# Kernel optimization log

Hardware: AMD Instinct MI355X
Metric: run time of the kernel (lower is better)

Reference implementation:

```python
import jax, jax.numpy as jnp
import numpy as np


def setup_inputs() -> dict:
    key = jax.random.key(0)
    k1, k2, k3 = jax.random.split(key, 3)
    B, T, C, F = 32, 4096, 256, 256
    scale = 1.0 / np.sqrt(2 * C)  # glorot-ish fan-in scaling for kernel_size=2
    return {
        "x": jax.random.normal(k1, (B, T, C), dtype=jnp.float32),
        "Wv": jax.random.normal(k2, (2, C, F), dtype=jnp.float32) * scale,
        "bv": jnp.zeros((F,), dtype=jnp.float32),
        "Wg": jax.random.normal(k3, (2, C, F), dtype=jnp.float32) * scale,
        "bg": jnp.zeros((F,), dtype=jnp.float32),
        "dilation": 4,
    }


def _causal_dilated_k2(x, W, b, d):
    # Causal Conv1D, kernel_size=2, dilation d: y[t] = x[t-d] @ W[0] + x[t] @ W[1] + b
    T = x.shape[1]
    x_prev = jnp.pad(x, ((0, 0), (d, 0), (0, 0)))[:, :T]  # left-pad with zeros
    return (jnp.einsum("btc,cf->btf", x_prev, W[0])
            + jnp.einsum("btc,cf->btf", x, W[1]) + b)


def reference(x, Wv, bv, Wg, bg, dilation):
    value = jnp.tanh(_causal_dilated_k2(x, Wv, bv, dilation))
    gate = jax.nn.sigmoid(_causal_dilated_k2(x, Wg, bg, dilation))
    activations = value * gate
    # gate_merge = Concatenate (channel axis by default in Keras for 3D tensors)
    return jnp.concatenate([activations, x], axis=-1)
```

## Files before the change

### kernel.cpp

```cpp
#include <hip/hip_runtime.h>
#include <hip/hip_bf16.h>
#include <cstdint>

#define B_    32
#define T_    4096
#define C_    256
#define BM    64
#define DMAX  16
#define NROWS (BM + DMAX)

typedef __attribute__((ext_vector_type(8))) short bf16x8;
typedef __attribute__((ext_vector_type(4))) float f32x4;
typedef __attribute__((ext_vector_type(4))) short s16x4;

static __device__ __forceinline__ short f2bf(float f) {
  __hip_bfloat16 h = __float2bfloat16(f);
  union { __hip_bfloat16 h; short s; } u; u.h = h;
  return u.s;
}

static __device__ __forceinline__ float rcp_(float x) {
  return __builtin_amdgcn_rcpf(x);
}

__global__ void prep_weights(const float* __restrict__ Wv, const float* __restrict__ Wg,
                             const float* __restrict__ bv, const float* __restrict__ bg,
                             short* __restrict__ wimg, float* __restrict__ bcat) {
  int id = blockIdx.x * 256 + threadIdx.x;
  int kk = id & 31;
  int np = (id >> 5) & 255;
  int ks = (id >> 13) & 15;
  int nb = id >> 17;
  int k = ks * 32 + kk, tap = k >> 8, kr = k & 255;
  int sel = np >> 7;
  int f = nb * 128 + (np & 127);
  const float* W = sel ? Wg : Wv;
  wimg[id] = f2bf(W[((size_t)tap * 256 + kr) * 256 + f]);
  if (id < 512) bcat[id] = (id < 256) ? bv[id] : bg[id - 256];
}

__global__ __launch_bounds__(512, 4) void snail_main(
    const float* __restrict__ x, const short* __restrict__ wimg,
    const float* __restrict__ bcat, const int* __restrict__ dptr,
    float* __restrict__ out) {
  __shared__ __align__(16) short lx[NROWS * C_];

  const int d = *dptr;
  const int bid = blockIdx.x;
  const int swz = (bid & 7) * 256 + (bid >> 3);
  const int t0 = (swz & 63) * BM;
  const int b  = swz >> 6;

  const int tid  = threadIdx.x;
  const int lane = tid & 63;
  const int w    = tid >> 6;
  const int nb   = w >> 2;
  const int wq   = w & 3;
  const int row15 = lane & 15;
  const int qw    = lane >> 4;

  const float* xb = x + (size_t)b * T_ * C_;
  float* ob = out + (size_t)b * T_ * 512;

  for (int i = tid; i < d * 64; i += 512) {
    int r = i >> 6, c4 = i & 63;
    int t = t0 - d + r;
    f32x4 v = (f32x4){0.f, 0.f, 0.f, 0.f};
    if (t >= 0) v = *(const f32x4*)(xb + (size_t)t * C_ + c4 * 4);
    s16x4 s;
    s.x = f2bf(v.x); s.y = f2bf(v.y); s.z = f2bf(v.z); s.w = f2bf(v.w);
    int byte = (r * 512 + c4 * 8) ^ ((r & 7) << 4);
    *(s16x4*)((char*)lx + byte) = s;
  }
#pragma unroll 4
  for (int ii = 0; ii < 8; ++ii) {
    int i = ii * 512 + tid;
    int rr = i >> 6, c4 = i & 63;
    int t = t0 + rr, r = rr + d;
    f32x4 v = *(const f32x4*)(xb + (size_t)t * C_ + c4 * 4);
    __builtin_nontemporal_store(v, (f32x4*)(ob + (size_t)t * 512 + C_ + c4 * 4));
    s16x4 s;
    s.x = f2bf(v.x); s.y = f2bf(v.y); s.z = f2bf(v.z); s.w = f2bf(v.w);
    int byte = (r * 512 + c4 * 8) ^ ((r & 7) << 4);
    *(s16x4*)((char*)lx + byte) = s;
  }
  __syncthreads();

  f32x4 accv[4][2], accg[4][2];
#pragma unroll
  for (int mi = 0; mi < 4; ++mi)
#pragma unroll
    for (int ni = 0; ni < 2; ++ni) {
      accv[mi][ni] = (f32x4){0.f, 0.f, 0.f, 0.f};
      accg[mi][ni] = (f32x4){0.f, 0.f, 0.f, 0.f};
    }

  const short* wl = wimg + (size_t)nb * 131072 + (wq * 32 + row15) * 32 + qw * 8;

#define LOADW(D0, D1, D2, D3, KS) do {                                  \
    const short* wk_ = wl + (KS) * 8192;                                \
    D0 = *(const bf16x8*)(wk_);                                         \
    D1 = *(const bf16x8*)(wk_ + 512);                                   \
    D2 = *(const bf16x8*)(wk_ + 4096);                                  \
    D3 = *(const bf16x8*)(wk_ + 4608);                                  \
  } while (0)

#define STEP(B0, B1, G0, G1, KS) do {                                   \
    bf16x8 af[4];                                                       \
    const int rofs_ = ((KS) >= 8) ? d : 0;                              \
    const int cb_ = ((KS) & 7) * 64 + qw * 16;                          \
    _Pragma("unroll")                                                   \
    for (int mi = 0; mi < 4; ++mi) {                                    \
      int r_ = 16 * mi + row15 + rofs_;                                 \
      af[mi] = *(const bf16x8*)((const char*)lx +                       \
               ((r_ * 512 + cb_) ^ ((r_ & 7) << 4)));                   \
    }                                                                   \
    _Pragma("unroll")                                                   \
    for (int mi = 0; mi < 4; ++mi) {                                    \
      accv[mi][0] = __builtin_amdgcn_mfma_f32_16x16x32_bf16(B0, af[mi], accv[mi][0], 0, 0, 0); \
      accv[mi][1] = __builtin_amdgcn_mfma_f32_16x16x32_bf16(B1, af[mi], accv[mi][1], 0, 0, 0); \
      accg[mi][0] = __builtin_amdgcn_mfma_f32_16x16x32_bf16(G0, af[mi], accg[mi][0], 0, 0, 0); \
      accg[mi][1] = __builtin_amdgcn_mfma_f32_16x16x32_bf16(G1, af[mi], accg[mi][1], 0, 0, 0); \
    }                                                                   \
  } while (0)

  bf16x8 a0, a1, a2, a3, b0, b1, b2, b3;
  LOADW(a0, a1, a2, a3, 0);
#pragma unroll 1
  for (int ks2 = 0; ks2 < 8; ++ks2) {
    LOADW(b0, b1, b2, b3, 2 * ks2 + 1);
    STEP(a0, a1, a2, a3, 2 * ks2);
    if (ks2 < 7) LOADW(a0, a1, a2, a3, 2 * ks2 + 2);
    STEP(b0, b1, b2, b3, 2 * ks2 + 1);
  }
#undef LOADW
#undef STEP

#pragma unroll
  for (int ni = 0; ni < 2; ++ni) {
    int f0 = nb * 128 + wq * 32 + 16 * ni + qw * 4;
    f32x4 bv4 = *(const f32x4*)(bcat + f0);
    f32x4 bg4 = *(const f32x4*)(bcat + 256 + f0);
    f32x4 bv2 = bv4 + bv4;
    f32x4 bgn = -bg4;
#pragma unroll
    for (int mi = 0; mi < 4; ++mi) {
      int t = t0 + 16 * mi + row15;
      f32x4 v = accv[mi][ni], g = accg[mi][ni];
      f32x4 res;
#pragma unroll
      for (int j = 0; j < 4; ++j) {
        float e2v = __expf(__builtin_fmaf(v[j], 2.f, bv2[j]));
        float eng = __expf(__builtin_fmaf(g[j], -1.f, bgn[j]));
        res[j] = (e2v - 1.f) * rcp_((e2v + 1.f) * (1.f + eng));
      }
      __builtin_nontemporal_store(res, (f32x4*)(ob + (size_t)t * 512 + f0));
    }
  }
}

extern "C" void kernel_launch(void* const* d_in, const int* in_sizes, int n_in,
                              void* d_out, int out_size, void* d_ws, size_t ws_size,
                              hipStream_t stream) {
  const float* x  = (const float*)d_in[0];
  const float* Wv = (const float*)d_in[1];
  const float* bv = (const float*)d_in[2];
  const float* Wg = (const float*)d_in[3];
  const float* bg = (const float*)d_in[4];
  const int* dil  = (const int*)d_in[5];
  float* out = (float*)d_out;

  short* wimg = (short*)d_ws;
  float* bcat = (float*)((char*)d_ws + 16 * 32768);

  prep_weights<<<1024, 256, 0, stream>>>(Wv, Wg, bv, bg, wimg, bcat);
  snail_main<<<B_ * (T_ / BM), 512, 0, stream>>>(x, wimg, bcat, dil, out);
}
```

Before: 110.4 us.

## Switch GEMM to 32x32x16 MFMA with per-wave 32-feature slices

Replaces the 16x16x32 bf16 MFMA tiling with 32x32x16 MFMA. Each of the 8 waves now owns 32 value and 32 gate features across all 64 time rows. The weight image is re-laid out to match the new fragment layout, and the K loop now runs 32 steps of 16. The goal is fewer MFMA instructions and fewer LDS A-fragment loads per FLOP. The cost is a different LDS access pattern and a changed epilogue write layout, which may cause more bank conflicts or less coalesced stores.

Result: slower. 173.1 us (+56.9%).

```diff
diff --git a/kernel.cpp b/kernel.cpp
--- a/kernel.cpp
+++ b/kernel.cpp
@@ -9,9 +9,10 @@
 #define DMAX  16
 #define NROWS (BM + DMAX)
 
-typedef __attribute__((ext_vector_type(8))) short bf16x8;
-typedef __attribute__((ext_vector_type(4))) float f32x4;
-typedef __attribute__((ext_vector_type(4))) short s16x4;
+typedef __attribute__((ext_vector_type(8)))  short bf16x8;
+typedef __attribute__((ext_vector_type(4)))  float f32x4;
+typedef __attribute__((ext_vector_type(16))) float f32x16;
+typedef __attribute__((ext_vector_type(4)))  short s16x4;
 
 static __device__ __forceinline__ short f2bf(float f) {
   __hip_bfloat16 h = __float2bfloat16(f);
@@ -27,13 +28,15 @@
                              const float* __restrict__ bv, const float* __restrict__ bg,
                              short* __restrict__ wimg, float* __restrict__ bcat) {
   int id = blockIdx.x * 256 + threadIdx.x;
-  int kk = id & 31;
-  int np = (id >> 5) & 255;
-  int ks = (id >> 13) & 15;
-  int nb = id >> 17;
-  int k = ks * 32 + kk, tap = k >> 8, kr = k & 255;
-  int sel = np >> 7;
-  int f = nb * 128 + (np & 127);
+  int j     = id & 7;
+  int lane6 = (id >> 3) & 63;
+  int blk   = (id >> 9) & 15;
+  int ks    = id >> 13;
+  int f5 = lane6 & 31, hi = lane6 >> 5;
+  int k = ks * 16 + hi * 8 + j;
+  int tap = k >> 8, kr = k & 255;
+  int sel = blk >> 3;
+  int f = (blk & 7) * 32 + f5;
   const float* W = sel ? Wg : Wv;
   wimg[id] = f2bf(W[((size_t)tap * 256 + kr) * 256 + f]);
   if (id < 512) bcat[id] = (id < 256) ? bv[id] : bg[id - 256];
@@ -54,10 +57,9 @@
   const int tid  = threadIdx.x;
   const int lane = tid & 63;
   const int w    = tid >> 6;
-  const int nb   = w >> 2;
-  const int wq   = w & 3;
-  const int row15 = lane & 15;
-  const int qw    = lane >> 4;
+  const int l31  = lane & 31;
+  const int hi   = lane >> 5;
+  const int hi16 = hi * 16;
 
   const float* xb = x + (size_t)b * T_ * C_;
   float* ob = out + (size_t)b * T_ * 512;
@@ -86,72 +88,64 @@
   }
   __syncthreads();
 
-  f32x4 accv[4][2], accg[4][2];
+  f32x16 accv[2], accg[2];
 #pragma unroll
-  for (int mi = 0; mi < 4; ++mi)
-#pragma unroll
-    for (int ni = 0; ni < 2; ++ni) {
-      accv[mi][ni] = (f32x4){0.f, 0.f, 0.f, 0.f};
-      accg[mi][ni] = (f32x4){0.f, 0.f, 0.f, 0.f};
-    }
+  for (int mi = 0; mi < 2; ++mi) {
+    accv[mi] = (f32x16)(0.f);
+    accg[mi] = (f32x16)(0.f);
+  }
 
-  const short* wl = wimg + (size_t)nb * 131072 + (wq * 32 + row15) * 32 + qw * 8;
+  const short* wbase = wimg + lane * 8;
 
-#define LOADW(D0, D1, D2, D3, KS) do {                                  \
-    const short* wk_ = wl + (KS) * 8192;                                \
-    D0 = *(const bf16x8*)(wk_);                                         \
-    D1 = *(const bf16x8*)(wk_ + 512);                                   \
-    D2 = *(const bf16x8*)(wk_ + 4096);                                  \
-    D3 = *(const bf16x8*)(wk_ + 4608);                                  \
+#define LOADW(WV, WG, KS) do {                                          \
+    WV = *(const bf16x8*)(wbase + (size_t)((KS) * 16 + w) * 512);       \
+    WG = *(const bf16x8*)(wbase + (size_t)((KS) * 16 + 8 + w) * 512);   \
   } while (0)
 
-#define STEP(B0, B1, G0, G1, KS) do {                                   \
-    bf16x8 af[4];                                                       \
-    const int rofs_ = ((KS) >= 8) ? d : 0;                              \
-    const int cb_ = ((KS) & 7) * 64 + qw * 16;                          \
+#define STEP(WV, WG, KS) do {                                           \
+    bf16x8 af[2];                                                       \
+    const int rofs_ = ((KS) >= 16) ? d : 0;                             \
+    const int cb_ = ((KS) & 15) * 32 + hi16;                            \
     _Pragma("unroll")                                                   \
-    for (int mi = 0; mi < 4; ++mi) {                                    \
-      int r_ = 16 * mi + row15 + rofs_;                                 \
+    for (int mi = 0; mi < 2; ++mi) {                                    \
+      int r_ = 32 * mi + l31 + rofs_;                                   \
       af[mi] = *(const bf16x8*)((const char*)lx +                       \
                ((r_ * 512 + cb_) ^ ((r_ & 7) << 4)));                   \
     }                                                                   \
     _Pragma("unroll")                                                   \
-    for (int mi = 0; mi < 4; ++mi) {                                    \
-      accv[mi][0] = __builtin_amdgcn_mfma_f32_16x16x32_bf16(B0, af[mi], accv[mi][0], 0, 0, 0); \
-      accv[mi][1] = __builtin_amdgcn_mfma_f32_16x16x32_bf16(B1, af[mi], accv[mi][1], 0, 0, 0); \
-      accg[mi][0] = __builtin_amdgcn_mfma_f32_16x16x32_bf16(G0, af[mi], accg[mi][0], 0, 0, 0); \
-      accg[mi][1] = __builtin_amdgcn_mfma_f32_16x16x32_bf16(G1, af[mi], accg[mi][1], 0, 0, 0); \
+    for (int mi = 0; mi < 2; ++mi) {                                    \
+      accv[mi] = __builtin_amdgcn_mfma_f32_32x32x16_bf16(WV, af[mi], accv[mi], 0, 0, 0); \
+      accg[mi] = __builtin_amdgcn_mfma_f32_32x32x16_bf16(WG, af[mi], accg[mi], 0, 0, 0); \
     }                                                                   \
   } while (0)
 
-  bf16x8 a0, a1, a2, a3, b0, b1, b2, b3;
-  LOADW(a0, a1, a2, a3, 0);
+  bf16x8 av, ag, bv_, bg_;
+  LOADW(av, ag, 0);
 #pragma unroll 1
-  for (int ks2 = 0; ks2 < 8; ++ks2) {
-    LOADW(b0, b1, b2, b3, 2 * ks2 + 1);
-    STEP(a0, a1, a2, a3, 2 * ks2);
-    if (ks2 < 7) LOADW(a0, a1, a2, a3, 2 * ks2 + 2);
-    STEP(b0, b1, b2, b3, 2 * ks2 + 1);
+  for (int ks2 = 0; ks2 < 16; ++ks2) {
+    LOADW(bv_, bg_, 2 * ks2 + 1);
+    STEP(av, ag, 2 * ks2);
+    if (ks2 < 15) LOADW(av, ag, 2 * ks2 + 2);
+    STEP(bv_, bg_, 2 * ks2 + 1);
   }
 #undef LOADW
 #undef STEP
 
 #pragma unroll
-  for (int ni = 0; ni < 2; ++ni) {
-    int f0 = nb * 128 + wq * 32 + 16 * ni + qw * 4;
-    f32x4 bv4 = *(const f32x4*)(bcat + f0);
-    f32x4 bg4 = *(const f32x4*)(bcat + 256 + f0);
-    f32x4 bv2 = bv4 + bv4;
-    f32x4 bgn = -bg4;
+  for (int mi = 0; mi < 2; ++mi) {
+    int t = t0 + 32 * mi + l31;
 #pragma unroll
-    for (int mi = 0; mi < 4; ++mi) {
-      int t = t0 + 16 * mi + row15;
-      f32x4 v = accv[mi][ni], g = accg[mi][ni];
+    for (int rg = 0; rg < 4; ++rg) {
+      int f0 = 32 * w + rg * 8 + 4 * hi;
+      f32x4 bv4 = *(const f32x4*)(bcat + f0);
+      f32x4 bg4 = *(const f32x4*)(bcat + 256 + f0);
       f32x4 res;
 #pragma unroll
       for (int j = 0; j < 4; ++j) {
-        float e2v = __expf(__builtin_fmaf(v[j], 2.f, bv2[j]));
-        float eng = __expf(__builtin_fmaf(g[j], -1.f, bgn[j]));
+        float vv = accv[mi][rg * 4 + j];
+        float gg = accg[mi][rg * 4 + j];
+        float e2v = __expf(__builtin_fmaf(vv, 2.f, bv4[j] + bv4[j]));
+        float eng = __expf(__builtin_fmaf(gg, -1.f, -bg4[j]));
         res[j] = (e2v - 1.f) * rcp_((e2v + 1.f) * (1.f + eng));
       }
       __builtin_nontemporal_store(res, (f32x4*)(ob + (size_t)t * 512 + f0));
```

## Warp-specialize loader waves to double-buffer x tiles across four time tiles

Applied to the files above, without the earlier changes.

Each block now handles four consecutive 64-row time tiles with 768 threads. Four extra waves stage the next tile's x (bf16 into LDS plus the fp32 passthrough copy) into a second LDS buffer while eight compute waves run the MFMA GEMM and gated activation on the current buffer. The aim is to hide global load latency behind compute and amortize per-block setup. In exchange DMAX drops to 8, which breaks dilations above 8. Per-tile barriers couple the producer and consumer waves, and the grid shrinks to 512 blocks, which may reduce occupancy.

Result: slower. 122.3 us (+10.8%).

```diff
diff --git a/kernel.cpp b/kernel.cpp
--- a/kernel.cpp
+++ b/kernel.cpp
@@ -6,8 +6,9 @@
 #define T_    4096
 #define C_    256
 #define BM    64
-#define DMAX  16
+#define DMAX  8
 #define NROWS (BM + DMAX)
+#define NT    4
 
 typedef __attribute__((ext_vector_type(8))) short bf16x8;
 typedef __attribute__((ext_vector_type(4))) float f32x4;
@@ -39,63 +40,50 @@
   if (id < 512) bcat[id] = (id < 256) ? bv[id] : bg[id - 256];
 }
 
-__global__ __launch_bounds__(512, 4) void snail_main(
+__global__ __launch_bounds__(768, 3) void snail_main(
     const float* __restrict__ x, const short* __restrict__ wimg,
     const float* __restrict__ bcat, const int* __restrict__ dptr,
     float* __restrict__ out) {
-  __shared__ __align__(16) short lx[NROWS * C_];
+  __shared__ __align__(16) short lx[2][NROWS * C_];
 
   const int d = *dptr;
   const int bid = blockIdx.x;
-  const int swz = (bid & 7) * 256 + (bid >> 3);
-  const int t0 = (swz & 63) * BM;
-  const int b  = swz >> 6;
+  const int swz = (bid & 7) * 64 + (bid >> 3);
+  const int b   = swz >> 4;
+  const int t00 = (swz & 15) * (NT * BM);
 
   const int tid  = threadIdx.x;
   const int lane = tid & 63;
   const int w    = tid >> 6;
-  const int nb   = w >> 2;
-  const int wq   = w & 3;
-  const int row15 = lane & 15;
-  const int qw    = lane >> 4;
 
   const float* xb = x + (size_t)b * T_ * C_;
   float* ob = out + (size_t)b * T_ * 512;
 
-  for (int i = tid; i < d * 64; i += 512) {
+  const int nrows = BM + d;
+
+  for (int i = tid; i < nrows * 64; i += 768) {
     int r = i >> 6, c4 = i & 63;
-    int t = t0 - d + r;
+    int t = t00 - d + r;
     f32x4 v = (f32x4){0.f, 0.f, 0.f, 0.f};
     if (t >= 0) v = *(const f32x4*)(xb + (size_t)t * C_ + c4 * 4);
+    if (r >= d)
+      __builtin_nontemporal_store(v, (f32x4*)(ob + (size_t)t * 512 + C_ + c4 * 4));
     s16x4 s;
     s.x = f2bf(v.x); s.y = f2bf(v.y); s.z = f2bf(v.z); s.w = f2bf(v.w);
     int byte = (r * 512 + c4 * 8) ^ ((r & 7) << 4);
-    *(s16x4*)((char*)lx + byte) = s;
-  }
-#pragma unroll 4
-  for (int ii = 0; ii < 8; ++ii) {
-    int i = ii * 512 + tid;
-    int rr = i >> 6, c4 = i & 63;
-    int t = t0 + rr, r = rr + d;
-    f32x4 v = *(const f32x4*)(xb + (size_t)t * C_ + c4 * 4);
-    __builtin_nontemporal_store(v, (f32x4*)(ob + (size_t)t * 512 + C_ + c4 * 4));
-    s16x4 s;
-    s.x = f2bf(v.x); s.y = f2bf(v.y); s.z = f2bf(v.z); s.w = f2bf(v.w);
-    int byte = (r * 512 + c4 * 8) ^ ((r & 7) << 4);
-    *(s16x4*)((char*)lx + byte) = s;
+    *(s16x4*)((char*)&lx[0][0] + byte) = s;
   }
   __syncthreads();
 
-  f32x4 accv[4][2], accg[4][2];
-#pragma unroll
-  for (int mi = 0; mi < 4; ++mi)
-#pragma unroll
-    for (int ni = 0; ni < 2; ++ni) {
-      accv[mi][ni] = (f32x4){0.f, 0.f, 0.f, 0.f};
-      accg[mi][ni] = (f32x4){0.f, 0.f, 0.f, 0.f};
-    }
-
-  const short* wl = wimg + (size_t)nb * 131072 + (wq * 32 + row15) * 32 + qw * 8;
+  if (w < 8) {
+    const int nb   = w >> 2;
+    const int wq   = w & 3;
+    const int row15 = lane & 15;
+    const int qw    = lane >> 4;
+
+    const short* wl = wimg + (size_t)nb * 131072 + (wq * 32 + row15) * 32 + qw * 8;
+
+    f32x4 accv[4][2], accg[4][2];
 
 #define LOADW(D0, D1, D2, D3, KS) do {                                  \
     const short* wk_ = wl + (KS) * 8192;                                \
@@ -105,14 +93,14 @@
     D3 = *(const bf16x8*)(wk_ + 4608);                                  \
   } while (0)
 
-#define STEP(B0, B1, G0, G1, KS) do {                                   \
+#define STEP(BASE, B0, B1, G0, G1, KS) do {                             \
     bf16x8 af[4];                                                       \
     const int rofs_ = ((KS) >= 8) ? d : 0;                              \
     const int cb_ = ((KS) & 7) * 64 + qw * 16;                          \
     _Pragma("unroll")                                                   \
     for (int mi = 0; mi < 4; ++mi) {                                    \
       int r_ = 16 * mi + row15 + rofs_;                                 \
-      af[mi] = *(const bf16x8*)((const char*)lx +                       \
+      af[mi] = *(const bf16x8*)((BASE) +                                \
                ((r_ * 512 + cb_) ^ ((r_ & 7) << 4)));                   \
     }                                                                   \
     _Pragma("unroll")                                                   \
@@ -124,37 +112,76 @@
     }                                                                   \
   } while (0)
 
-  bf16x8 a0, a1, a2, a3, b0, b1, b2, b3;
-  LOADW(a0, a1, a2, a3, 0);
 #pragma unroll 1
-  for (int ks2 = 0; ks2 < 8; ++ks2) {
-    LOADW(b0, b1, b2, b3, 2 * ks2 + 1);
-    STEP(a0, a1, a2, a3, 2 * ks2);
-    if (ks2 < 7) LOADW(a0, a1, a2, a3, 2 * ks2 + 2);
-    STEP(b0, b1, b2, b3, 2 * ks2 + 1);
-  }
+    for (int tt = 0; tt < NT; ++tt) {
+      const int t0 = t00 + tt * BM;
+      const char* base = (const char*)&lx[tt & 1][0];
+
+#pragma unroll
+      for (int mi = 0; mi < 4; ++mi)
+#pragma unroll
+        for (int ni = 0; ni < 2; ++ni) {
+          accv[mi][ni] = (f32x4){0.f, 0.f, 0.f, 0.f};
+          accg[mi][ni] = (f32x4){0.f, 0.f, 0.f, 0.f};
+        }
+
+      bf16x8 a0, a1, a2, a3, b0, b1, b2, b3;
+      LOADW(a0, a1, a2, a3, 0);
+#pragma unroll 1
+      for (int ks2 = 0; ks2 < 8; ++ks2) {
+        LOADW(b0, b1, b2, b3, 2 * ks2 + 1);
+        STEP(base, a0, a1, a2, a3, 2 * ks2);
+        if (ks2 < 7) LOADW(a0, a1, a2, a3, 2 * ks2 + 2);
+        STEP(base, b0, b1, b2, b3, 2 * ks2 + 1);
+      }
+
+      __syncthreads();
+
+#pragma unroll
+      for (int ni = 0; ni < 2; ++ni) {
+        int f0 = nb * 128 + wq * 32 + 16 * ni + qw * 4;
+        f32x4 bv4 = *(const f32x4*)(bcat + f0);
+        f32x4 bg4 = *(const f32x4*)(bcat + 256 + f0);
+        f32x4 bv2 = bv4 + bv4;
+        f32x4 bgn = -bg4;
+#pragma unroll
+        for (int mi = 0; mi < 4; ++mi) {
+          int t = t0 + 16 * mi + row15;
+          f32x4 v = accv[mi][ni], g = accg[mi][ni];
+          f32x4 res;
+#pragma unroll
+          for (int j = 0; j < 4; ++j) {
+            float e2v = __expf(__builtin_fmaf(v[j], 2.f, bv2[j]));
+            float eng = __expf(__builtin_fmaf(g[j], -1.f, bgn[j]));
+            res[j] = (e2v - 1.f) * rcp_((e2v + 1.f) * (1.f + eng));
+          }
+          __builtin_nontemporal_store(res, (f32x4*)(ob + (size_t)t * 512 + f0));
+        }
+      }
+    }
 #undef LOADW
 #undef STEP
-
-#pragma unroll
-  for (int ni = 0; ni < 2; ++ni) {
-    int f0 = nb * 128 + wq * 32 + 16 * ni + qw * 4;
-    f32x4 bv4 = *(const f32x4*)(bcat + f0);
-    f32x4 bg4 = *(const f32x4*)(bcat + 256 + f0);
-    f32x4 bv2 = bv4 + bv4;
-    f32x4 bgn = -bg4;
-#pragma unroll
-    for (int mi = 0; mi < 4; ++mi) {
-      int t = t0 + 16 * mi + row15;
-      f32x4 v = accv[mi][ni], g = accg[mi][ni];
-      f32x4 res;
-#pragma unroll
-      for (int j = 0; j < 4; ++j) {
-        float e2v = __expf(__builtin_fmaf(v[j], 2.f, bv2[j]));
-        float eng = __expf(__builtin_fmaf(g[j], -1.f, bgn[j]));
-        res[j] = (e2v - 1.f) * rcp_((e2v + 1.f) * (1.f + eng));
+  } else {
+    const int st = tid - 512;
+#pragma unroll 1
+    for (int tt = 0; tt < NT; ++tt) {
+      if (tt < NT - 1) {
+        const int tb = t00 + (tt + 1) * BM;
+        char* dst = (char*)&lx[(tt + 1) & 1][0];
+#pragma unroll 2
+        for (int i = st; i < nrows * 64; i += 256) {
+          int r = i >> 6, c4 = i & 63;
+          int t = tb - d + r;
+          f32x4 v = *(const f32x4*)(xb + (size_t)t * C_ + c4 * 4);
+          if (r >= d)
+            __builtin_nontemporal_store(v, (f32x4*)(ob + (size_t)t * 512 + C_ + c4 * 4));
+          s16x4 s;
+          s.x = f2bf(v.x); s.y = f2bf(v.y); s.z = f2bf(v.z); s.w = f2bf(v.w);
+          int byte = (r * 512 + c4 * 8) ^ ((r & 7) << 4);
+          *(s16x4*)(dst + byte) = s;
+        }
       }
-      __builtin_nontemporal_store(res, (f32x4*)(ob + (size_t)t * 512 + f0));
+      __syncthreads();
     }
   }
 }
@@ -174,5 +201,5 @@
   float* bcat = (float*)((char*)d_ws + 16 * 32768);
 
   prep_weights<<<1024, 256, 0, stream>>>(Wv, Wg, bv, bg, wimg, bcat);
-  snail_main<<<B_ * (T_ / BM), 512, 0, stream>>>(x, wimg, bcat, dil, out);
-}
+  snail_main<<<B_ * (T_ / BM) / NT, 768, 0, stream>>>(x, wimg, bcat, dil, out);
+}
```
